# Optimization experiments

Hardware: AMD Instinct MI355X
Metric: run time of the kernel (lower is better)

## Reference

```python
import jax, jax.numpy as jnp
import numpy as np

# --- SLAYER-style constants (network.yaml defaults) ---
T_BINS = 350      # tSample / Ts
TS = 1.0          # simulation time step
THETA = 10.0      # spike threshold
TAU_SR = 10.0     # SRM (psp) kernel time constant
TAU_REF = 1.0     # refractory kernel time constant
SCALE_REF = 2.0
TAU_RHO = 1.0     # surrogate-gradient width (unused in fwd)
SCALE_RHO = 1.0
REF_LEN = 32      # truncated refractory kernel length
B = 32            # batch

_t = jnp.arange(T_BINS, dtype=jnp.float32) * TS
SRM_KERNEL = (_t / TAU_SR) * jnp.exp(1.0 - _t / TAU_SR)            # alpha kernel, peak 1 at t=tauSr
_tr = jnp.arange(REF_LEN, dtype=jnp.float32) * TS
REF_KERNEL = -SCALE_REF * THETA * (_tr / TAU_REF) * jnp.exp(1.0 - _tr / TAU_REF)


def psp(x):
    # causal temporal convolution with SRM kernel; x: [B, N, T]
    b, n, t = x.shape
    k = SRM_KERNEL[::-1].reshape(1, 1, T_BINS)  # flip: lax conv is cross-correlation
    y = jax.lax.conv_general_dilated(x.reshape(b * n, 1, t), k, (1,), [(T_BINS - 1, 0)])
    return y.reshape(b, n, t)


def _spike_fwd_impl(u):
    # threshold + refractory dynamics, serial over time; u: [B, N, T]
    uT = jnp.moveaxis(u, -1, 0)  # [T, B, N]
    def step(buf, ut):
        v = ut + buf[..., 0]                       # membrane + pending refractory
        s = (v >= THETA).astype(u.dtype)           # 0/1 spike indicator
        buf = jnp.concatenate([buf[..., 1:], jnp.zeros_like(buf[..., :1])], axis=-1) \
              + s[..., None] * REF_KERNEL
        return buf, s / TS
    buf0 = jnp.zeros(u.shape[:-1] + (REF_LEN,), u.dtype)
    _, sT = jax.lax.scan(step, buf0, uT)
    return jnp.moveaxis(sT, 0, -1)


@jax.custom_vjp
def spike(u):
    return _spike_fwd_impl(u)

def _spike_f(u):
    return _spike_fwd_impl(u), u

def _spike_b(u, g):
    # SLAYER surrogate gradient: pdf of spiking
    pdf = (SCALE_RHO / TAU_RHO) * jnp.exp(-jnp.abs(u - THETA) / TAU_RHO)
    return (g * pdf,)

spike.defvjp(_spike_f, _spike_b)


def encode(inp, table):
    # vectorized pixel->time-bin one-hot scatter (replaces the Python quadruple loop)
    t_idx = table[inp]                                   # gather: [B,3,32,32]
    return jax.nn.one_hot(t_idx, T_BINS, dtype=jnp.float32) / TS  # [B,3,32,32,T]


def setup_inputs() -> dict:
    key = jax.random.key(0)
    k1, k2, k3 = jax.random.split(key, 3)
    inp = jax.random.randint(k1, (B, 3, 32, 32), 0, 256, dtype=jnp.int32)
    table = ((jnp.arange(256) * T_BINS) // 256).astype(jnp.int32)  # pixel value -> time bin
    w1 = jax.random.normal(k2, (240, 3 * 32 * 32), dtype=jnp.float32)
    w2 = jax.random.normal(k3, (10, 240), dtype=jnp.float32)
    return {"inp": inp, "table": table, "w1": w1, "w2": w2}


def reference(inp, table, w1, w2):
    spikes = encode(inp, table).reshape(inp.shape[0], -1, T_BINS)      # [B,3072,T]
    l1 = spike(psp(jnp.einsum('bpt,np->bnt', spikes, w1)))             # [B,240,T]
    l2 = spike(psp(jnp.einsum('bpt,np->bnt', l1, w2)))                 # [B,10,T]
    return l2
```

## Files before the change

### kernel.cpp

```cpp
#include <hip/hip_runtime.h>
#include <math.h>

#define T_BINS 350
#define REF_LEN 32
#define NB 32
#define NPIX 3072
#define N1 240
#define N2 10
#define NVAL 256

__global__ void prep(const int* __restrict__ inp,
                     int* __restrict__ pix,
                     int* __restrict__ offs,
                     int* __restrict__ cnts,
                     const float* __restrict__ w1,
                     float* __restrict__ w1t,
                     const int* __restrict__ table,
                     int* __restrict__ inv)
{
    __shared__ int lc[NVAL];
    __shared__ int ls[NVAL];
    __shared__ int lslot[NVAL];
    __shared__ float tile[64][65];
    __shared__ int linv[T_BINS];

    const int tid = threadIdx.x;

    if (blockIdx.x < NB) {
        const int b = blockIdx.x;
        lc[tid] = 0;
        __syncthreads();

        int vals[12];
        #pragma unroll
        for (int i = 0; i < 12; ++i) {
            int v = inp[b * NPIX + i * 256 + tid];
            vals[i] = v;
            atomicAdd(&lc[v], 1);
        }
        __syncthreads();

        int x = lc[tid];
        ls[tid] = x;
        __syncthreads();
        for (int d = 1; d < 256; d <<= 1) {
            int y = (tid >= d) ? ls[tid - d] : 0;
            __syncthreads();
            ls[tid] += y;
            __syncthreads();
        }
        int excl = ls[tid] - x;
        offs[b * NVAL + tid] = excl;
        cnts[b * NVAL + tid] = x;
        lslot[tid] = excl;
        __syncthreads();

        #pragma unroll
        for (int i = 0; i < 12; ++i) {
            int slot = atomicAdd(&lslot[vals[i]], 1);
            pix[b * NPIX + slot] = i * 256 + tid;
        }
    } else if (blockIdx.x < NB + 192) {
        const int tt = blockIdx.x - NB;
        const int p0 = (tt % 48) * 64;
        const int n0 = (tt / 48) * 64;
        const int c  = tid & 63;
        const int r0 = tid >> 6;

        #pragma unroll
        for (int i = 0; i < 16; ++i) {
            int n = n0 + r0 + i * 4;
            if (n < N1) tile[r0 + i * 4][c] = w1[n * NPIX + p0 + c];
        }
        __syncthreads();
        #pragma unroll
        for (int i = 0; i < 16; ++i) {
            int p = p0 + r0 + i * 4;
            int n = n0 + c;
            if (n < N1) w1t[p * N1 + n] = tile[c][r0 + i * 4];
        }
    } else {
        for (int i = tid; i < T_BINS; i += 256) linv[i] = -1;
        __syncthreads();
        if (tid < NVAL) linv[table[tid]] = tid;
        __syncthreads();
        for (int i = tid; i < T_BINS; i += 256) inv[i] = linv[i];
    }
}

__global__ void compute_u1(const float* __restrict__ w1t,
                           const int* __restrict__ pix,
                           const int* __restrict__ offs,
                           const int* __restrict__ cnts,
                           const int* __restrict__ inv,
                           float* __restrict__ u1t)
{
    const int t = blockIdx.x;
    const int b = blockIdx.y;
    const int tid = threadIdx.x;
    if (tid >= N1) return;
    const int v = inv[t];

    double acc = 0.0;
    if (v >= 0) {
        const int cnt = cnts[b * NVAL + v];
        const int* pl = pix + b * NPIX + offs[b * NVAL + v];
        int i = 0;
        for (; i + 4 <= cnt; i += 4) {
            int p0 = pl[i], p1 = pl[i + 1], p2 = pl[i + 2], p3 = pl[i + 3];
            double w0 = (double)w1t[p0 * N1 + tid];
            double w1v = (double)w1t[p1 * N1 + tid];
            double w2v = (double)w1t[p2 * N1 + tid];
            double w3 = (double)w1t[p3 * N1 + tid];
            acc += w0; acc += w1v; acc += w2v; acc += w3;
        }
        for (; i < cnt; ++i)
            acc += (double)w1t[pl[i] * N1 + tid];
    }
    u1t[((size_t)b * T_BINS + t) * N1 + tid] = (float)acc;
}

#define DYN_CONSTS \
    const double A    = 0.9048374180359595;     \
    const double C    = 0.2718281828459045;     \
    const double Ar   = 0.36787944117144233;    \
    const double Cr   = -54.365636569180904;    \
    const double C31A = 1.0671679036256927e-12; \
    const double C31B = 3.4424771084699765e-14;

#define DYN_CORE(uin)                                         \
        q = A * (q + p);                                      \
        p = A * p + (uin);                                    \
        double vm = C * q + Cr * Q;                           \
        unsigned int sb = (vm >= 10.0) ? 1u : 0u;             \
        double s = (double)sb;                                \
        double sel31 = (hist & 0x80000000u) ? C31A : 0.0;     \
        double sel30 = (hist & 0x40000000u) ? C31B : 0.0;     \
        Q = Ar * (Q + P - sel31);                             \
        P = s + (Ar * P - sel30);                             \
        hist = (hist << 1) | sb;

__global__ __launch_bounds__(64) void layer1_dyn(
                           const float* __restrict__ u1t,
                           unsigned long long* __restrict__ s1m)
{
    const int tid = threadIdx.x;
    const int b   = blockIdx.x >> 2;
    const int k   = blockIdx.x & 3;
    const int n   = k * 64 + tid;
    if (n >= N1) return;

    const float* ub = u1t + (size_t)b * T_BINS * N1 + n;
    unsigned long long* mp = s1m + ((size_t)b * T_BINS) * 4 + k;

    DYN_CONSTS
    double p = 0.0, q = 0.0, P = 0.0, Q = 0.0;
    unsigned int hist = 0u;

    double cb[14], nb[14];
    #pragma unroll
    for (int i = 0; i < 14; ++i) cb[i] = (double)ub[(size_t)i * N1];

    for (int t0 = 0; t0 < T_BINS; t0 += 14) {
        if (t0 + 14 < T_BINS) {
            #pragma unroll
            for (int i = 0; i < 14; ++i)
                nb[i] = (double)ub[(size_t)(t0 + 14 + i) * N1];
        }
        #pragma unroll
        for (int i = 0; i < 14; ++i) {
            DYN_CORE(cb[i])
            unsigned long long msk = __ballot(sb != 0u);
            if (tid == 0) mp[(size_t)(t0 + i) * 4] = msk;
        }
        #pragma unroll
        for (int i = 0; i < 14; ++i) cb[i] = nb[i];
    }
}

__global__ void compute_u2(const unsigned long long* __restrict__ s1m,
                           const float* __restrict__ w2,
                           float* __restrict__ u2)
{
    __shared__ float lw2[N2][N1];
    const int tid = threadIdx.x;
    for (int i = tid; i < N2 * N1; i += 256) lw2[i / N1][i % N1] = w2[i];
    __syncthreads();

    int id = blockIdx.x * 256 + tid;
    if (id >= NB * T_BINS * N2) return;
    int bt = id / N2;
    int m  = id - bt * N2;
    const unsigned long long* mp = s1m + (size_t)bt * 4;

    double acc = 0.0;
    #pragma unroll
    for (int kk = 0; kk < 4; ++kk) {
        unsigned long long msk = mp[kk];
        while (msk) {
            int j = __ffsll(msk) - 1;
            acc += (double)lw2[m][kk * 64 + j];
            msk &= msk - 1;
        }
    }
    u2[id] = (float)acc;
}

__global__ void layer2_dyn(const float* __restrict__ u2,
                           float* __restrict__ out)
{
    const int id = blockIdx.x * 64 + threadIdx.x;
    if (id >= NB * N2) return;
    const int b = id / N2;
    const int m = id - b * N2;
    const float* up = u2 + (size_t)b * T_BINS * N2 + m;
    float*       op = out + ((size_t)b * N2 + m) * T_BINS;

    DYN_CONSTS
    double p = 0.0, q = 0.0, P = 0.0, Q = 0.0;
    unsigned int hist = 0u;

    double cb[14], nb[14];
    #pragma unroll
    for (int i = 0; i < 14; ++i) cb[i] = (double)up[(size_t)i * N2];

    for (int t0 = 0; t0 < T_BINS; t0 += 14) {
        if (t0 + 14 < T_BINS) {
            #pragma unroll
            for (int i = 0; i < 14; ++i)
                nb[i] = (double)up[(size_t)(t0 + 14 + i) * N2];
        }
        #pragma unroll
        for (int i = 0; i < 14; ++i) {
            DYN_CORE(cb[i])
            op[t0 + i] = (float)s;
        }
        #pragma unroll
        for (int i = 0; i < 14; ++i) cb[i] = nb[i];
    }
}

extern "C" void kernel_launch(void* const* d_in, const int* in_sizes, int n_in,
                              void* d_out, int out_size, void* d_ws, size_t ws_size,
                              hipStream_t stream) {
    const int*   inp   = (const int*)d_in[0];
    const int*   table = (const int*)d_in[1];
    const float* w1    = (const float*)d_in[2];
    const float* w2    = (const float*)d_in[3];
    float* out = (float*)d_out;

    char* ws = (char*)d_ws;
    size_t off = 0;
    float* u1t = (float*)(ws + off);  off += (size_t)NB * T_BINS * N1 * 4;
    float* u2  = (float*)(ws + off);  off += (size_t)NB * T_BINS * N2 * 4;
    float* w1t = (float*)(ws + off);  off += (size_t)NPIX * N1 * 4;
    unsigned long long* s1m = (unsigned long long*)(ws + off);
    off += (size_t)NB * T_BINS * 4 * 8;
    int*   pix = (int*)(ws + off);    off += (size_t)NB * NPIX * 4;
    int*  offs = (int*)(ws + off);    off += (size_t)NB * NVAL * 4;
    int*  cnts = (int*)(ws + off);    off += (size_t)NB * NVAL * 4;
    int*   inv = (int*)(ws + off);    off += (size_t)T_BINS * 4;

    prep<<<NB + 192 + 1, 256, 0, stream>>>(inp, pix, offs, cnts, w1, w1t, table, inv);
    compute_u1<<<dim3(T_BINS, NB), 256, 0, stream>>>(w1t, pix, offs, cnts, inv, u1t);
    layer1_dyn<<<NB * 4, 64, 0, stream>>>(u1t, s1m);
    compute_u2<<<(NB * T_BINS * N2 + 255) / 256, 256, 0, stream>>>(s1m, w2, u2);
    layer2_dyn<<<(NB * N2 + 63) / 64, 64, 0, stream>>>(u2, out);
}
```

Baseline: 150.1 us.

## Fuse layer-1 dynamics, layer-2 projection and layer-2 dynamics into one per-batch kernel

Layer-1 input is now computed per pixel value (256 values) instead of per time bin, and the dynamics kernel gathers it through the inverse table on the fly. The layer-1 dynamics, spike-mask matvec with w2 and layer-2 dynamics are fused into one block per batch, with masks and u2 kept in shared memory. This removes two kernel launches and the global round trips for u1t, s1m and u2. In exchange the fused kernel runs only 32 blocks, the gathered W reads are irregular, and the layer-2 serial scan uses just 10 threads per block.

```diff
diff --git a/kernel.cpp b/kernel.cpp
--- a/kernel.cpp
+++ b/kernel.cpp
@@ -88,36 +88,34 @@
     }
 }
 
-__global__ void compute_u1(const float* __restrict__ w1t,
-                           const int* __restrict__ pix,
-                           const int* __restrict__ offs,
-                           const int* __restrict__ cnts,
-                           const int* __restrict__ inv,
-                           float* __restrict__ u1t)
+__global__ void compute_w(const float* __restrict__ w1t,
+                          const int* __restrict__ pix,
+                          const int* __restrict__ offs,
+                          const int* __restrict__ cnts,
+                          float* __restrict__ W)
 {
-    const int t = blockIdx.x;
-    const int b = blockIdx.y;
+    const int b   = blockIdx.y;
     const int tid = threadIdx.x;
     if (tid >= N1) return;
-    const int v = inv[t];
-
-    double acc = 0.0;
-    if (v >= 0) {
+
+    for (int vv = 0; vv < 4; ++vv) {
+        const int v = blockIdx.x * 4 + vv;
         const int cnt = cnts[b * NVAL + v];
         const int* pl = pix + b * NPIX + offs[b * NVAL + v];
+        double acc = 0.0;
         int i = 0;
         for (; i + 4 <= cnt; i += 4) {
             int p0 = pl[i], p1 = pl[i + 1], p2 = pl[i + 2], p3 = pl[i + 3];
-            double w0 = (double)w1t[p0 * N1 + tid];
+            double w0  = (double)w1t[p0 * N1 + tid];
             double w1v = (double)w1t[p1 * N1 + tid];
             double w2v = (double)w1t[p2 * N1 + tid];
-            double w3 = (double)w1t[p3 * N1 + tid];
+            double w3  = (double)w1t[p3 * N1 + tid];
             acc += w0; acc += w1v; acc += w2v; acc += w3;
         }
         for (; i < cnt; ++i)
             acc += (double)w1t[pl[i] * N1 + tid];
-    }
-    u1t[((size_t)b * T_BINS + t) * N1 + tid] = (float)acc;
+        W[((size_t)b * NVAL + v) * N1 + tid] = (float)acc;
+    }
 }
 
 #define DYN_CONSTS \
@@ -140,103 +138,109 @@
         P = s + (Ar * P - sel30);                             \
         hist = (hist << 1) | sb;
 
-__global__ __launch_bounds__(64) void layer1_dyn(
-                           const float* __restrict__ u1t,
-                           unsigned long long* __restrict__ s1m)
+__global__ __launch_bounds__(256) void fused_dyn(
+        const float* __restrict__ W,
+        const int* __restrict__ inv,
+        const float* __restrict__ w2,
+        float* __restrict__ out)
 {
-    const int tid = threadIdx.x;
-    const int b   = blockIdx.x >> 2;
-    const int k   = blockIdx.x & 3;
-    const int n   = k * 64 + tid;
-    if (n >= N1) return;
-
-    const float* ub = u1t + (size_t)b * T_BINS * N1 + n;
-    unsigned long long* mp = s1m + ((size_t)b * T_BINS) * 4 + k;
-
-    DYN_CONSTS
-    double p = 0.0, q = 0.0, P = 0.0, Q = 0.0;
-    unsigned int hist = 0u;
-
-    double cb[14], nb[14];
-    #pragma unroll
-    for (int i = 0; i < 14; ++i) cb[i] = (double)ub[(size_t)i * N1];
-
-    for (int t0 = 0; t0 < T_BINS; t0 += 14) {
-        if (t0 + 14 < T_BINS) {
-            #pragma unroll
-            for (int i = 0; i < 14; ++i)
-                nb[i] = (double)ub[(size_t)(t0 + 14 + i) * N1];
-        }
+    __shared__ unsigned long long smask[T_BINS][4];
+    __shared__ float lw2[N2][N1];
+    __shared__ float su2[T_BINS][N2];
+    __shared__ int linv[T_BINS];
+
+    const int tid  = threadIdx.x;
+    const int b    = blockIdx.x;
+    const int k    = tid >> 6;
+    const int lane = tid & 63;
+    const int n    = k * 64 + lane;
+
+    for (int i = tid; i < N2 * N1; i += 256) lw2[i / N1][i % N1] = w2[i];
+    for (int i = tid; i < T_BINS; i += 256) linv[i] = inv[i];
+    __syncthreads();
+
+    {
+        DYN_CONSTS
+        double p = 0.0, q = 0.0, P = 0.0, Q = 0.0;
+        unsigned int hist = 0u;
+        const bool valid = (n < N1);
+        const float* Wb = W + (size_t)b * NVAL * N1 + (valid ? n : 0);
+
+        double cb[14], nb[14];
         #pragma unroll
         for (int i = 0; i < 14; ++i) {
-            DYN_CORE(cb[i])
-            unsigned long long msk = __ballot(sb != 0u);
-            if (tid == 0) mp[(size_t)(t0 + i) * 4] = msk;
-        }
-        #pragma unroll
-        for (int i = 0; i < 14; ++i) cb[i] = nb[i];
-    }
-}
-
-__global__ void compute_u2(const unsigned long long* __restrict__ s1m,
-                           const float* __restrict__ w2,
-                           float* __restrict__ u2)
-{
-    __shared__ float lw2[N2][N1];
-    const int tid = threadIdx.x;
-    for (int i = tid; i < N2 * N1; i += 256) lw2[i / N1][i % N1] = w2[i];
-    __syncthreads();
-
-    int id = blockIdx.x * 256 + tid;
-    if (id >= NB * T_BINS * N2) return;
-    int bt = id / N2;
-    int m  = id - bt * N2;
-    const unsigned long long* mp = s1m + (size_t)bt * 4;
-
-    double acc = 0.0;
-    #pragma unroll
-    for (int kk = 0; kk < 4; ++kk) {
-        unsigned long long msk = mp[kk];
-        while (msk) {
-            int j = __ffsll(msk) - 1;
-            acc += (double)lw2[m][kk * 64 + j];
-            msk &= msk - 1;
-        }
-    }
-    u2[id] = (float)acc;
-}
-
-__global__ void layer2_dyn(const float* __restrict__ u2,
-                           float* __restrict__ out)
-{
-    const int id = blockIdx.x * 64 + threadIdx.x;
-    if (id >= NB * N2) return;
-    const int b = id / N2;
-    const int m = id - b * N2;
-    const float* up = u2 + (size_t)b * T_BINS * N2 + m;
-    float*       op = out + ((size_t)b * N2 + m) * T_BINS;
-
-    DYN_CONSTS
-    double p = 0.0, q = 0.0, P = 0.0, Q = 0.0;
-    unsigned int hist = 0u;
-
-    double cb[14], nb[14];
-    #pragma unroll
-    for (int i = 0; i < 14; ++i) cb[i] = (double)up[(size_t)i * N2];
-
-    for (int t0 = 0; t0 < T_BINS; t0 += 14) {
-        if (t0 + 14 < T_BINS) {
-            #pragma unroll
-            for (int i = 0; i < 14; ++i)
-                nb[i] = (double)up[(size_t)(t0 + 14 + i) * N2];
-        }
-        #pragma unroll
-        for (int i = 0; i < 14; ++i) {
-            DYN_CORE(cb[i])
-            op[t0 + i] = (float)s;
-        }
-        #pragma unroll
-        for (int i = 0; i < 14; ++i) cb[i] = nb[i];
+            int v = linv[i];
+            cb[i] = (valid && v >= 0) ? (double)Wb[(size_t)v * N1] : 0.0;
+        }
+
+        for (int t0 = 0; t0 < T_BINS; t0 += 14) {
+            if (t0 + 14 < T_BINS) {
+                #pragma unroll
+                for (int i = 0; i < 14; ++i) {
+                    int v = linv[t0 + 14 + i];
+                    nb[i] = (valid && v >= 0) ? (double)Wb[(size_t)v * N1] : 0.0;
+                }
+            }
+            #pragma unroll
+            for (int i = 0; i < 14; ++i) {
+                DYN_CORE(cb[i])
+                unsigned long long msk = __ballot(sb != 0u);
+                if (lane == 0) smask[t0 + i][k] = msk;
+            }
+            #pragma unroll
+            for (int i = 0; i < 14; ++i) cb[i] = nb[i];
+        }
+    }
+    __syncthreads();
+
+    for (int id = tid; id < T_BINS * N2; id += 256) {
+        const int t = id / N2;
+        const int m = id - t * N2;
+        double acc = 0.0;
+        #pragma unroll
+        for (int kk = 0; kk < 4; ++kk) {
+            unsigned long long msk = smask[t][kk];
+            while (msk) {
+                int j = __ffsll(msk) - 1;
+                acc += (double)lw2[m][kk * 64 + j];
+                msk &= msk - 1;
+            }
+        }
+        su2[t][m] = (float)acc;
+    }
+    __syncthreads();
+
+    if (tid < N2) {
+        const int m = tid;
+        DYN_CONSTS
+        double p = 0.0, q = 0.0, P = 0.0, Q = 0.0;
+        unsigned int hist = 0u;
+
+        double cb[14], nb[14];
+        #pragma unroll
+        for (int i = 0; i < 14; ++i) cb[i] = (double)su2[i][m];
+
+        for (int t0 = 0; t0 < T_BINS; t0 += 14) {
+            if (t0 + 14 < T_BINS) {
+                #pragma unroll
+                for (int i = 0; i < 14; ++i) nb[i] = (double)su2[t0 + 14 + i][m];
+            }
+            #pragma unroll
+            for (int i = 0; i < 14; ++i) {
+                DYN_CORE(cb[i])
+                su2[t0 + i][m] = (float)s;
+            }
+            #pragma unroll
+            for (int i = 0; i < 14; ++i) cb[i] = nb[i];
+        }
+    }
+    __syncthreads();
+
+    float* ob = out + (size_t)b * N2 * T_BINS;
+    for (int id = tid; id < N2 * T_BINS; id += 256) {
+        const int m = id / T_BINS;
+        const int t = id - m * T_BINS;
+        ob[id] = su2[t][m];
     }
 }
 
@@ -251,19 +255,14 @@
 
     char* ws = (char*)d_ws;
     size_t off = 0;
-    float* u1t = (float*)(ws + off);  off += (size_t)NB * T_BINS * N1 * 4;
-    float* u2  = (float*)(ws + off);  off += (size_t)NB * T_BINS * N2 * 4;
+    float* W   = (float*)(ws + off);  off += (size_t)NB * NVAL * N1 * 4;
     float* w1t = (float*)(ws + off);  off += (size_t)NPIX * N1 * 4;
-    unsigned long long* s1m = (unsigned long long*)(ws + off);
-    off += (size_t)NB * T_BINS * 4 * 8;
     int*   pix = (int*)(ws + off);    off += (size_t)NB * NPIX * 4;
     int*  offs = (int*)(ws + off);    off += (size_t)NB * NVAL * 4;
     int*  cnts = (int*)(ws + off);    off += (size_t)NB * NVAL * 4;
     int*   inv = (int*)(ws + off);    off += (size_t)T_BINS * 4;
 
     prep<<<NB + 192 + 1, 256, 0, stream>>>(inp, pix, offs, cnts, w1, w1t, table, inv);
-    compute_u1<<<dim3(T_BINS, NB), 256, 0, stream>>>(w1t, pix, offs, cnts, inv, u1t);
-    layer1_dyn<<<NB * 4, 64, 0, stream>>>(u1t, s1m);
-    compute_u2<<<(NB * T_BINS * N2 + 255) / 256, 256, 0, stream>>>(s1m, w2, u2);
-    layer2_dyn<<<(NB * N2 + 63) / 64, 64, 0, stream>>>(u2, out);
-}
+    compute_w<<<dim3(NVAL / 4, NB), 256, 0, stream>>>(w1t, pix, offs, cnts, W);
+    fused_dyn<<<NB, 256, 0, stream>>>(W, inv, w2, out);
+}
```

After: 231.7 us. 54.4% more time.
